# Performance work log

Hardware: AMD Instinct MI355X
Metric: run time of the kernel (lower is better)

The kernel has to match this reference:

```python
import jax, jax.numpy as jnp
import numpy as np

# Dimensions matching init_kwargs
O = 4096   # out_features
I = 4096   # in_features
R = 32     # svd_rank
G = 64     # n_groups
GS = I // G  # group_size = 64
NBITS = 4
NUM_BYTES = O * I * NBITS // 8


def setup_inputs() -> dict:
    key = jax.random.key(0)
    ks = jax.random.split(key, 7)
    return {
        "x": jax.random.normal(ks[0], (1, 4096, I), dtype=jnp.float32),
        # bit-packed int4 weights, two nibbles per byte (stored as int32 holding 0..255)
        "w_packed": jax.random.randint(ks[1], (NUM_BYTES,), 0, 256, dtype=jnp.int32),
        "svd_up": jax.random.normal(ks[2], (O, R), dtype=jnp.float32) * 0.02,
        "svd_down": jax.random.normal(ks[3], (R, I), dtype=jnp.float32) * 0.02,
        "scale": jax.random.uniform(ks[4], (O, G, 1), dtype=jnp.float32, minval=0.001, maxval=0.02),
        "zero_point": jax.random.uniform(ks[5], (O, G, 1), dtype=jnp.float32, minval=0.0, maxval=15.0),
        "bias": jax.random.normal(ks[6], (O,), dtype=jnp.float32) * 0.01,
    }


def _dequantize(w_packed, svd_up, svd_down, scale, zero_point):
    # Unpack two 4-bit values per byte (low nibble first).
    low = w_packed & 0xF
    high = (w_packed >> 4) & 0xF
    w_q = jnp.stack([low, high], axis=-1).reshape(O, G, GS).astype(jnp.float32)
    # Per-group affine dequant: (q - zero) * scale, then SVD low-rank correction.
    W = ((w_q - zero_point) * scale).reshape(O, I)
    return W + svd_up @ svd_down  # [O, I]


def reference(x, w_packed, svd_up, svd_down, scale, zero_point, bias):
    # forward_int8 path (tokens > 16, int8_matmul=True)
    W_f = _dequantize(w_packed, svd_up, svd_down, scale, zero_point).T  # [I, O]
    xm = x.reshape(-1, I)  # [N, I]
    # Dynamic per-row activation quant
    scale_x = jnp.max(jnp.abs(xm), axis=1, keepdims=True) / 127.0  # [N, 1]
    x_q = jnp.clip(jnp.round(xm / scale_x), -128, 127).astype(jnp.int8)
    # Dynamic per-column weight quant
    scale_w = jnp.max(jnp.abs(W_f), axis=0, keepdims=True) / 127.0  # [1, O]
    W_q = jnp.clip(jnp.round(W_f / scale_w), -128, 127).astype(jnp.int8)
    # int8 GEMM with int32 accumulation, then dequant scales + bias
    acc = jnp.matmul(x_q.astype(jnp.int32), W_q.astype(jnp.int32))  # [N, O] int32
    out = acc.astype(jnp.float32) * scale_x * scale_w + bias
    return out.reshape(*x.shape[:-1], O)
```

## Files before the change

kernel.cpp:

```cpp
#include <hip/hip_runtime.h>
#include <cstdint>
#include <cstddef>

#define I_DIM 4096
#define O_DIM 4096
#define RNK 32
#define NGRP 64
#define N_TOK 4096

typedef int v4i __attribute__((ext_vector_type(4)));

__device__ __forceinline__ int clamp_i8(float v) {
    int q = (int)rintf(v);
    q = q < -128 ? -128 : q;
    q = q > 127 ? 127 : q;
    return q;
}

#define BO 8

__global__ __launch_bounds__(256) void quant_w_kernel(
    const int* __restrict__ w_packed, const float* __restrict__ svd_up,
    const float* __restrict__ svd_down, const float* __restrict__ scale,
    const float* __restrict__ zp, char* __restrict__ w_q,
    float* __restrict__ scale_w)
{
    __shared__ float s_up[BO][RNK];
    __shared__ float s_sc[BO][NGRP];
    __shared__ float s_zp[BO][NGRP];
    __shared__ float s_red[BO][4];
    __shared__ float s_sw[BO];

    const int tid = threadIdx.x;
    const int o0 = blockIdx.x * BO;

    s_up[tid >> 5][tid & 31] = svd_up[(size_t)(o0 + (tid >> 5)) * RNK + (tid & 31)];
    for (int t = tid; t < BO * NGRP; t += 256) {
        s_sc[t >> 6][t & 63] = scale[(size_t)(o0 + (t >> 6)) * NGRP + (t & 63)];
        s_zp[t >> 6][t & 63] = zp[(size_t)(o0 + (t >> 6)) * NGRP + (t & 63)];
    }
    __syncthreads();

    float vmax[BO];
#pragma unroll
    for (int ro = 0; ro < BO; ro++) vmax[ro] = 0.0f;

    for (int j = 0; j < 8; j++) {
        const int p = tid + 256 * j;
        const int i = 2 * p;
        const int g = i >> 6;
        float c0[BO], c1[BO];
#pragma unroll
        for (int ro = 0; ro < BO; ro++) { c0[ro] = 0.0f; c1[ro] = 0.0f; }
#pragma unroll 4
        for (int r = 0; r < RNK; r++) {
            const float2 d = *(const float2*)&svd_down[(size_t)r * I_DIM + i];
#pragma unroll
            for (int ro = 0; ro < BO; ro++) {
                c0[ro] += s_up[ro][r] * d.x;
                c1[ro] += s_up[ro][r] * d.y;
            }
        }
#pragma unroll
        for (int ro = 0; ro < BO; ro++) {
            const int b = w_packed[(size_t)(o0 + ro) * (I_DIM / 2) + p];
            const float sc = s_sc[ro][g], z = s_zp[ro][g];
            const float w0 = ((float)(b & 0xF) - z) * sc + c0[ro];
            const float w1 = ((float)((b >> 4) & 0xF) - z) * sc + c1[ro];
            vmax[ro] = fmaxf(vmax[ro], fmaxf(fabsf(w0), fabsf(w1)));
        }
    }

    const int lane = tid & 63, wv = tid >> 6;
#pragma unroll
    for (int ro = 0; ro < BO; ro++) {
        float m = vmax[ro];
        for (int off = 32; off > 0; off >>= 1)
            m = fmaxf(m, __shfl_down(m, off, 64));
        if (lane == 0) s_red[ro][wv] = m;
    }
    __syncthreads();
    if (tid < BO) {
        const float m = fmaxf(fmaxf(s_red[tid][0], s_red[tid][1]),
                              fmaxf(s_red[tid][2], s_red[tid][3]));
        const float sw = m / 127.0f;
        scale_w[o0 + tid] = sw;
        s_sw[tid] = sw;
    }
    __syncthreads();

    for (int j = 0; j < 8; j++) {
        const int p = tid + 256 * j;
        const int i = 2 * p;
        const int g = i >> 6;
        float c0[BO], c1[BO];
#pragma unroll
        for (int ro = 0; ro < BO; ro++) { c0[ro] = 0.0f; c1[ro] = 0.0f; }
#pragma unroll 4
        for (int r = 0; r < RNK; r++) {
            const float2 d = *(const float2*)&svd_down[(size_t)r * I_DIM + i];
#pragma unroll
            for (int ro = 0; ro < BO; ro++) {
                c0[ro] += s_up[ro][r] * d.x;
                c1[ro] += s_up[ro][r] * d.y;
            }
        }
#pragma unroll
        for (int ro = 0; ro < BO; ro++) {
            const int b = w_packed[(size_t)(o0 + ro) * (I_DIM / 2) + p];
            const float sc = s_sc[ro][g], z = s_zp[ro][g];
            const float w0 = ((float)(b & 0xF) - z) * sc + c0[ro];
            const float w1 = ((float)((b >> 4) & 0xF) - z) * sc + c1[ro];
            const float sw = s_sw[ro];
            const int q0 = clamp_i8(w0 / sw);
            const int q1 = clamp_i8(w1 / sw);
            ((short*)w_q)[(size_t)(o0 + ro) * (I_DIM / 2) + p] =
                (short)((q0 & 0xFF) | ((q1 & 0xFF) << 8));
        }
    }
}

__global__ __launch_bounds__(256) void quant_x_kernel(
    const float* __restrict__ x, char* __restrict__ x_q,
    float* __restrict__ scale_x)
{
    const int n = blockIdx.x;
    const int tid = threadIdx.x;
    const float4* xr = (const float4*)(x + (size_t)n * I_DIM);
    float4 v[4];
    float m = 0.0f;
#pragma unroll
    for (int j = 0; j < 4; j++) {
        v[j] = xr[tid + 256 * j];
        m = fmaxf(m, fmaxf(fmaxf(fabsf(v[j].x), fabsf(v[j].y)),
                           fmaxf(fabsf(v[j].z), fabsf(v[j].w))));
    }
    __shared__ float s_red[4];
    __shared__ float s_sx;
    for (int off = 32; off > 0; off >>= 1)
        m = fmaxf(m, __shfl_down(m, off, 64));
    if ((tid & 63) == 0) s_red[tid >> 6] = m;
    __syncthreads();
    if (tid == 0) {
        const float mm = fmaxf(fmaxf(s_red[0], s_red[1]),
                               fmaxf(s_red[2], s_red[3]));
        const float sx = mm / 127.0f;
        scale_x[n] = sx;
        s_sx = sx;
    }
    __syncthreads();
    const float sx = s_sx;
    int* outw = (int*)(x_q + (size_t)n * I_DIM);
#pragma unroll
    for (int j = 0; j < 4; j++) {
        const int q0 = clamp_i8(v[j].x / sx);
        const int q1 = clamp_i8(v[j].y / sx);
        const int q2 = clamp_i8(v[j].z / sx);
        const int q3 = clamp_i8(v[j].w / sx);
        outw[tid + 256 * j] =
            (q0 & 0xFF) | ((q1 & 0xFF) << 8) | ((q2 & 0xFF) << 16) | ((q3 & 0xFF) << 24);
    }
}

#define BM 128
#define BN 128
#define BK 128

__global__ __launch_bounds__(256) void gemm_i8_kernel(
    const char* __restrict__ x_q, const char* __restrict__ w_q,
    const float* __restrict__ scale_x, const float* __restrict__ scale_w,
    const float* __restrict__ bias, float* __restrict__ out)
{
    __shared__ v4i As4[BM * BK / 16];
    __shared__ v4i Bs4[BN * BK / 16];
    char* As = (char*)As4;
    char* Bs = (char*)Bs4;

    const int tid = threadIdx.x;
    const int bm0 = blockIdx.x * BM;
    const int bn0 = blockIdx.y * BN;
    const int lane = tid & 63, wv = tid >> 6;
    const int wm = wv & 1, wn = wv >> 1;
    const int quad = lane >> 4, l15 = lane & 15;

    v4i acc[4][4];
#pragma unroll
    for (int mt = 0; mt < 4; mt++)
#pragma unroll
        for (int nt = 0; nt < 4; nt++)
            acc[mt][nt] = (v4i){0, 0, 0, 0};

    for (int kk = 0; kk < I_DIM / BK; kk++) {
        const int k0 = kk * BK;
#pragma unroll
        for (int j = 0; j < 4; j++) {
            const int c = tid + 256 * j;
            const int row = c >> 3;
            const int kc = (c & 7) ^ (row & 7);
            const char* ga = x_q + (size_t)(bm0 + row) * I_DIM + k0 + kc * 16;
            __builtin_amdgcn_global_load_lds(
                (const __attribute__((address_space(1))) unsigned int*)ga,
                (__attribute__((address_space(3))) unsigned int*)(As + c * 16),
                16, 0, 0);
            const char* gb = w_q + (size_t)(bn0 + row) * I_DIM + k0 + kc * 16;
            __builtin_amdgcn_global_load_lds(
                (const __attribute__((address_space(1))) unsigned int*)gb,
                (__attribute__((address_space(3))) unsigned int*)(Bs + c * 16),
                16, 0, 0);
        }
        __syncthreads();
#pragma unroll
        for (int s = 0; s < 2; s++) {
            v4i af[4], bf[4];
#pragma unroll
            for (int mt = 0; mt < 4; mt++) {
                const int row = wm * 64 + mt * 16 + l15;
                const int kc = (s * 4 + quad) ^ (l15 & 7);
                af[mt] = *(const v4i*)(As + row * BK + kc * 16);
            }
#pragma unroll
            for (int nt = 0; nt < 4; nt++) {
                const int row = wn * 64 + nt * 16 + l15;
                const int kc = (s * 4 + quad) ^ (l15 & 7);
                bf[nt] = *(const v4i*)(Bs + row * BK + kc * 16);
            }
#pragma unroll
            for (int mt = 0; mt < 4; mt++)
#pragma unroll
                for (int nt = 0; nt < 4; nt++)
                    acc[mt][nt] = __builtin_amdgcn_mfma_i32_16x16x64_i8(
                        af[mt], bf[nt], acc[mt][nt], 0, 0, 0);
        }
        __syncthreads();
    }

#pragma unroll
    for (int mt = 0; mt < 4; mt++) {
        const int n0 = bm0 + wm * 64 + mt * 16 + quad * 4;
        float sx[4];
#pragma unroll
        for (int r = 0; r < 4; r++) sx[r] = scale_x[n0 + r];
#pragma unroll
        for (int nt = 0; nt < 4; nt++) {
            const int oc = bn0 + wn * 64 + nt * 16 + l15;
            const float sw = scale_w[oc];
            const float bs = bias[oc];
#pragma unroll
            for (int r = 0; r < 4; r++) {
                out[(size_t)(n0 + r) * O_DIM + oc] =
                    (float)acc[mt][nt][r] * sx[r] * sw + bs;
            }
        }
    }
}

extern "C" void kernel_launch(void* const* d_in, const int* in_sizes, int n_in,
                              void* d_out, int out_size, void* d_ws, size_t ws_size,
                              hipStream_t stream) {
    const float* x        = (const float*)d_in[0];
    const int*   w_packed = (const int*)d_in[1];
    const float* svd_up   = (const float*)d_in[2];
    const float* svd_down = (const float*)d_in[3];
    const float* scale    = (const float*)d_in[4];
    const float* zp       = (const float*)d_in[5];
    const float* bias     = (const float*)d_in[6];
    float* out = (float*)d_out;

    char* ws = (char*)d_ws;
    char*  w_q     = ws;
    char*  x_q     = ws + ((size_t)16 << 20);
    float* scale_w = (float*)(ws + ((size_t)32 << 20));
    float* scale_x = (float*)(ws + ((size_t)32 << 20) + 16384);

    quant_w_kernel<<<O_DIM / BO, 256, 0, stream>>>(w_packed, svd_up, svd_down,
                                                   scale, zp, w_q, scale_w);
    quant_x_kernel<<<N_TOK, 256, 0, stream>>>(x, x_q, scale_x);
    gemm_i8_kernel<<<dim3(N_TOK / BM, O_DIM / BN), 256, 0, stream>>>(
        x_q, w_q, scale_x, scale_w, bias, out);
}
```

Baseline: 294.8 us.

## Keep dequantized weights in registers to avoid recomputing low-rank correction

The weight quantization kernel now computes each dequantized weight (nibble affine plus the SVD low-rank term) once, holds it in registers across the max-reduction, and reuses it for the int8 quantization pass instead of recomputing everything. Rows per block drop from 8 to 4 to fit the register array, with wider int2/float4/int32 loads and stores and a multiply by a reciprocal in place of division. svd_up is read straight from global memory rather than staged in shared memory. The costs are higher register pressure, more blocks reading svd_down, and possible last-bit differences from the reciprocal multiply.

```diff
diff --git a/kernel.cpp b/kernel.cpp
--- a/kernel.cpp
+++ b/kernel.cpp
@@ -17,15 +17,14 @@
     return q;
 }
 
-#define BO 8
-
-__global__ __launch_bounds__(256) void quant_w_kernel(
+#define BO 4
+
+__global__ __launch_bounds__(256, 4) void quant_w_kernel(
     const int* __restrict__ w_packed, const float* __restrict__ svd_up,
     const float* __restrict__ svd_down, const float* __restrict__ scale,
     const float* __restrict__ zp, char* __restrict__ w_q,
     float* __restrict__ scale_w)
 {
-    __shared__ float s_up[BO][RNK];
     __shared__ float s_sc[BO][NGRP];
     __shared__ float s_zp[BO][NGRP];
     __shared__ float s_red[BO][4];
@@ -34,40 +33,51 @@
     const int tid = threadIdx.x;
     const int o0 = blockIdx.x * BO;
 
-    s_up[tid >> 5][tid & 31] = svd_up[(size_t)(o0 + (tid >> 5)) * RNK + (tid & 31)];
     for (int t = tid; t < BO * NGRP; t += 256) {
         s_sc[t >> 6][t & 63] = scale[(size_t)(o0 + (t >> 6)) * NGRP + (t & 63)];
         s_zp[t >> 6][t & 63] = zp[(size_t)(o0 + (t >> 6)) * NGRP + (t & 63)];
     }
     __syncthreads();
 
+    float W[4][BO][4];
     float vmax[BO];
 #pragma unroll
     for (int ro = 0; ro < BO; ro++) vmax[ro] = 0.0f;
 
-    for (int j = 0; j < 8; j++) {
-        const int p = tid + 256 * j;
-        const int i = 2 * p;
-        const int g = i >> 6;
-        float c0[BO], c1[BO];
-#pragma unroll
-        for (int ro = 0; ro < BO; ro++) { c0[ro] = 0.0f; c1[ro] = 0.0f; }
+#pragma unroll
+    for (int jq = 0; jq < 4; jq++) {
+        const int q = tid + 256 * jq;
+        const int i = 4 * q;
+        const int g = q >> 4;
+
+#pragma unroll
+        for (int ro = 0; ro < BO; ro++) {
+            const int2 b2 = *(const int2*)&w_packed[(size_t)(o0 + ro) * (I_DIM / 2) + 2 * q];
+            const float sc = s_sc[ro][g], z = s_zp[ro][g];
+            W[jq][ro][0] = ((float)(b2.x & 0xF) - z) * sc;
+            W[jq][ro][1] = ((float)((b2.x >> 4) & 0xF) - z) * sc;
+            W[jq][ro][2] = ((float)(b2.y & 0xF) - z) * sc;
+            W[jq][ro][3] = ((float)((b2.y >> 4) & 0xF) - z) * sc;
+        }
+
 #pragma unroll 4
         for (int r = 0; r < RNK; r++) {
-            const float2 d = *(const float2*)&svd_down[(size_t)r * I_DIM + i];
+            const float4 d = *(const float4*)&svd_down[(size_t)r * I_DIM + i];
 #pragma unroll
             for (int ro = 0; ro < BO; ro++) {
-                c0[ro] += s_up[ro][r] * d.x;
-                c1[ro] += s_up[ro][r] * d.y;
-            }
-        }
+                const float u = svd_up[(size_t)(o0 + ro) * RNK + r];
+                W[jq][ro][0] += u * d.x;
+                W[jq][ro][1] += u * d.y;
+                W[jq][ro][2] += u * d.z;
+                W[jq][ro][3] += u * d.w;
+            }
+        }
+
 #pragma unroll
         for (int ro = 0; ro < BO; ro++) {
-            const int b = w_packed[(size_t)(o0 + ro) * (I_DIM / 2) + p];
-            const float sc = s_sc[ro][g], z = s_zp[ro][g];
-            const float w0 = ((float)(b & 0xF) - z) * sc + c0[ro];
-            const float w1 = ((float)((b >> 4) & 0xF) - z) * sc + c1[ro];
-            vmax[ro] = fmaxf(vmax[ro], fmaxf(fabsf(w0), fabsf(w1)));
+            vmax[ro] = fmaxf(vmax[ro],
+                fmaxf(fmaxf(fabsf(W[jq][ro][0]), fabsf(W[jq][ro][1])),
+                      fmaxf(fabsf(W[jq][ro][2]), fabsf(W[jq][ro][3]))));
         }
     }
 
@@ -89,33 +99,21 @@
     }
     __syncthreads();
 
-    for (int j = 0; j < 8; j++) {
-        const int p = tid + 256 * j;
-        const int i = 2 * p;
-        const int g = i >> 6;
-        float c0[BO], c1[BO];
-#pragma unroll
-        for (int ro = 0; ro < BO; ro++) { c0[ro] = 0.0f; c1[ro] = 0.0f; }
-#pragma unroll 4
-        for (int r = 0; r < RNK; r++) {
-            const float2 d = *(const float2*)&svd_down[(size_t)r * I_DIM + i];
-#pragma unroll
-            for (int ro = 0; ro < BO; ro++) {
-                c0[ro] += s_up[ro][r] * d.x;
-                c1[ro] += s_up[ro][r] * d.y;
-            }
-        }
+    float inv[BO];
+#pragma unroll
+    for (int ro = 0; ro < BO; ro++) inv[ro] = 1.0f / s_sw[ro];
+
+#pragma unroll
+    for (int jq = 0; jq < 4; jq++) {
+        const int q = tid + 256 * jq;
 #pragma unroll
         for (int ro = 0; ro < BO; ro++) {
-            const int b = w_packed[(size_t)(o0 + ro) * (I_DIM / 2) + p];
-            const float sc = s_sc[ro][g], z = s_zp[ro][g];
-            const float w0 = ((float)(b & 0xF) - z) * sc + c0[ro];
-            const float w1 = ((float)((b >> 4) & 0xF) - z) * sc + c1[ro];
-            const float sw = s_sw[ro];
-            const int q0 = clamp_i8(w0 / sw);
-            const int q1 = clamp_i8(w1 / sw);
-            ((short*)w_q)[(size_t)(o0 + ro) * (I_DIM / 2) + p] =
-                (short)((q0 & 0xFF) | ((q1 & 0xFF) << 8));
+            const int q0 = clamp_i8(W[jq][ro][0] * inv[ro]);
+            const int q1 = clamp_i8(W[jq][ro][1] * inv[ro]);
+            const int q2 = clamp_i8(W[jq][ro][2] * inv[ro]);
+            const int q3 = clamp_i8(W[jq][ro][3] * inv[ro]);
+            ((int*)w_q)[(size_t)(o0 + ro) * (I_DIM / 4) + q] =
+                (q0 & 0xFF) | ((q1 & 0xFF) << 8) | ((q2 & 0xFF) << 16) | ((q3 & 0xFF) << 24);
         }
     }
 }
```

New measurement: 254.7 us. 1.16x faster.
